# Kernel optimization log

Hardware: AMD Instinct MI355X
Metric: run time of the kernel (lower is better)

## Reference

```python
import jax, jax.numpy as jnp
import numpy as np
import math

B, T = 2, 1024
D_MODEL = 1024
N_HEAD = 16
HEAD_DIM = D_MODEL // N_HEAD
VOCAB = 32000
NUM_LOOP = 4
EPS_LN = 1e-5                       # torch LayerNorm default
EPS_RMS = float(np.finfo(np.float32).eps)  # torch RMSNorm eps=None -> finfo eps


def setup_inputs() -> dict:
    key = jax.random.key(0)
    ks = jax.random.split(key, 12)
    s = 0.02
    d = D_MODEL
    tok = jax.random.normal(ks[1], (VOCAB, d), jnp.float32) * s
    tok = tok.at[0].set(0.0)  # padding_idx=0
    return {
        "idx": jax.random.randint(ks[0], (B, T), 0, VOCAB),
        "tok_embed": tok,
        "ln_e_g": jnp.ones((d,), jnp.float32),
        "ln_e_b": jnp.zeros((d,), jnp.float32),
        "Wqkv": jax.random.normal(ks[2], (d, 3 * d), jnp.float32) * s,
        "bqkv": jnp.zeros((3 * d,), jnp.float32),
        "Wo": jax.random.normal(ks[3], (d, d), jnp.float32) * s,
        "bo": jnp.zeros((d,), jnp.float32),
        "W1": jax.random.normal(ks[4], (d, 4 * d), jnp.float32) * s,
        "b1": jnp.zeros((4 * d,), jnp.float32),
        "W2": jax.random.normal(ks[5], (4 * d, d), jnp.float32) * s,
        "b2": jnp.zeros((d,), jnp.float32),
        "n1_w": jnp.ones((d,), jnp.float32),
        "n2_w": jnp.ones((d,), jnp.float32),
        "lnf_g": jnp.ones((d,), jnp.float32),
        "lnf_b": jnp.zeros((d,), jnp.float32),
        "Wlm": jax.random.normal(ks[6], (d, VOCAB), jnp.float32) * s,
        "blm": jnp.zeros((VOCAB,), jnp.float32),
    }


def layernorm(x, g, b):
    m = jnp.mean(x, axis=-1, keepdims=True)
    v = jnp.mean(jnp.square(x - m), axis=-1, keepdims=True)
    return (x - m) * jax.lax.rsqrt(v + EPS_LN) * g + b


def rmsnorm(x, w):
    ms = jnp.mean(jnp.square(x), axis=-1, keepdims=True)
    return x * jax.lax.rsqrt(ms + EPS_RMS) * w


def gelu_tanh(x):
    c = math.sqrt(2.0 / math.pi)
    return 0.5 * x * (1.0 + jnp.tanh(c * (x + 0.044715 * x * x * x)))


def alibi_causal_bias(t):
    # rpe[q,k] = -(q-k) for q>k else 0, scaled per head by 2^(-8/H*(h+1)); causal -inf above diag
    pos = jnp.arange(t)
    rel = pos[:, None] - pos[None, :]                      # [T,T] = q - k
    slopes = 2.0 ** (-8.0 / N_HEAD * jnp.arange(1, N_HEAD + 1, dtype=jnp.float32))
    bias = -slopes[:, None, None] * rel.astype(jnp.float32)  # [H,T,T]
    return jnp.where(rel[None] >= 0, bias, -jnp.inf)       # causal mask fused


def reference(idx, tok_embed, ln_e_g, ln_e_b, Wqkv, bqkv, Wo, bo,
              W1, b1, W2, b2, n1_w, n2_w, lnf_g, lnf_b, Wlm, blm):
    b, t = idx.shape
    x = layernorm(tok_embed[idx], ln_e_g, ln_e_b)          # rpe=True: no sinusoidal PE
    bias = alibi_causal_bias(t)                            # [H,T,T]
    scale = 1.0 / math.sqrt(HEAD_DIM)

    for _ in range(NUM_LOOP):
        # attention sublayer
        h = rmsnorm(x, n1_w)
        qkv = h @ Wqkv + bqkv
        q, k, v = jnp.split(qkv, 3, axis=-1)
        q = q.reshape(b, t, N_HEAD, HEAD_DIM).transpose(0, 2, 1, 3)
        k = k.reshape(b, t, N_HEAD, HEAD_DIM).transpose(0, 2, 1, 3)
        v = v.reshape(b, t, N_HEAD, HEAD_DIM).transpose(0, 2, 1, 3)
        att = jnp.einsum('bhqd,bhkd->bhqk', q, k) * scale + bias[None]
        att = jax.nn.softmax(att, axis=-1)
        y = jnp.einsum('bhqk,bhkd->bhqd', att, v)
        y = y.transpose(0, 2, 1, 3).reshape(b, t, D_MODEL)
        x = x + (y @ Wo + bo)
        # mlp sublayer
        h = rmsnorm(x, n2_w)
        x = x + (gelu_tanh(h @ W1 + b1) @ W2 + b2)

    x = layernorm(x, lnf_g, lnf_b)
    return x @ Wlm + blm  # [B,T,VOCAB]
```

## Files before the change

### kernel.cpp

```cpp
#include <hip/hip_runtime.h>
#include <stdint.h>

#define DEVI __device__ __forceinline__

typedef __attribute__((ext_vector_type(8))) short short8;
typedef __attribute__((ext_vector_type(4))) float f32x4;
typedef unsigned short u16;
typedef unsigned int u32;

typedef const __attribute__((address_space(1))) void* gas_ptr;
typedef __attribute__((address_space(3))) void* las_ptr;

constexpr int BBATCH = 2;
constexpr int TT  = 1024;
constexpr int BT  = BBATCH * TT;
constexpr int DM  = 1024;
constexpr int NH  = 16;
constexpr int HD  = 64;
constexpr int DFF = 4096;
constexpr int NV  = 32000;
constexpr int NL  = 4;

DEVI u16 f2b(float f) {
  u32 u = __builtin_bit_cast(u32, f);
  u = (u + 0x7fffu + ((u >> 16) & 1u)) >> 16;
  return (u16)u;
}
DEVI float b2f(u16 h) { return __builtin_bit_cast(float, (u32)h << 16); }

DEVI void gld16(const void* g, void* l) {
  __builtin_amdgcn_global_load_lds((gas_ptr)g, (las_ptr)l, 16, 0, 0);
}

DEVI float wave_sum(float v) {
#pragma unroll
  for (int off = 32; off; off >>= 1) v += __shfl_xor(v, off);
  return v;
}
DEVI float block_sum(float v, float* sb) {
  v = wave_sum(v);
  int lane = threadIdx.x & 63, wid = threadIdx.x >> 6;
  __syncthreads();
  if (lane == 0) sb[wid] = v;
  __syncthreads();
  return sb[0] + sb[1] + sb[2] + sb[3];
}

DEVI float gelu_f(float x) {
  float u = 0.7978845608028654f * (x + 0.044715f * x * x * x);
  float e = __expf(2.0f * u);
  return x * (1.0f - 1.0f / (e + 1.0f));
}

__global__ __launch_bounds__(256) void wt_transpose_all(
    const float* __restrict__ Wqkv, const float* __restrict__ Wo,
    const float* __restrict__ W1, const float* __restrict__ W2,
    const float* __restrict__ Wlm,
    u16* __restrict__ WqkvT, u16* __restrict__ WoT, u16* __restrict__ W1T,
    u16* __restrict__ W2T, u16* __restrict__ WlmT) {
  __shared__ float t[64][33];
  int bid = blockIdx.x;
  const float* in; u16* out; int K, N, tt;
  if (bid < 1536)      { in = Wqkv; out = WqkvT; K = 1024; N = 3072;  tt = bid; }
  else if (bid < 2048) { in = Wo;   out = WoT;   K = 1024; N = 1024;  tt = bid - 1536; }
  else if (bid < 4096) { in = W1;   out = W1T;   K = 1024; N = 4096;  tt = bid - 2048; }
  else if (bid < 6144) { in = W2;   out = W2T;   K = 4096; N = 1024;  tt = bid - 4096; }
  else                 { in = Wlm;  out = WlmT;  K = 1024; N = 32000; tt = bid - 6144; }
  int nx = N >> 5;
  int n0 = (tt % nx) * 32, k0 = (tt / nx) * 64;
  int tx = threadIdx.x & 31, ty = threadIdx.x >> 5;
#pragma unroll
  for (int i = 0; i < 8; ++i)
    t[ty + 8 * i][tx] = in[(size_t)(k0 + ty + 8 * i) * N + n0 + tx];
  __syncthreads();
#pragma unroll
  for (int i = 0; i < 4; ++i) {
    int r = ty + 8 * i;
    u32 pk = (u32)f2b(t[2 * tx][r]) | ((u32)f2b(t[2 * tx + 1][r]) << 16);
    *(u32*)(out + (size_t)(n0 + r) * K + k0 + 2 * tx) = pk;
  }
}

__global__ __launch_bounds__(256) void embed_ln_k(const int* __restrict__ idx,
                                                  const float* __restrict__ tok,
                                                  const float* __restrict__ g,
                                                  const float* __restrict__ b,
                                                  float* __restrict__ x) {
  __shared__ float sb[4];
  int row = blockIdx.x, tid = threadIdx.x;
  float4 v = ((const float4*)(tok + (size_t)idx[row] * DM))[tid];
  float s = block_sum(v.x + v.y + v.z + v.w, sb);
  float m = s * (1.0f / DM);
  float dx = v.x - m, dy = v.y - m, dz = v.z - m, dw = v.w - m;
  float q = block_sum(dx * dx + dy * dy + dz * dz + dw * dw, sb);
  float rs = rsqrtf(q * (1.0f / DM) + 1e-5f);
  float4 gg = ((const float4*)g)[tid];
  float4 bb = ((const float4*)b)[tid];
  float4 o = make_float4(dx * rs * gg.x + bb.x, dy * rs * gg.y + bb.y,
                         dz * rs * gg.z + bb.z, dw * rs * gg.w + bb.w);
  ((float4*)(x + (size_t)row * DM))[tid] = o;
}

__global__ __launch_bounds__(256) void final_ln_k(const float* __restrict__ x,
                                                  const float* __restrict__ g,
                                                  const float* __restrict__ b,
                                                  u16* __restrict__ xf) {
  __shared__ float sb[4];
  int row = blockIdx.x, tid = threadIdx.x;
  float4 v = ((const float4*)(x + (size_t)row * DM))[tid];
  float s = block_sum(v.x + v.y + v.z + v.w, sb);
  float m = s * (1.0f / DM);
  float dx = v.x - m, dy = v.y - m, dz = v.z - m, dw = v.w - m;
  float q = block_sum(dx * dx + dy * dy + dz * dz + dw * dw, sb);
  float rs = rsqrtf(q * (1.0f / DM) + 1e-5f);
  float4 gg = ((const float4*)g)[tid];
  float4 bb = ((const float4*)b)[tid];
  u32 lo = (u32)f2b(dx * rs * gg.x + bb.x) | ((u32)f2b(dy * rs * gg.y + bb.y) << 16);
  u32 hi = (u32)f2b(dz * rs * gg.z + bb.z) | ((u32)f2b(dw * rs * gg.w + bb.w) << 16);
  ((uint2*)(xf + (size_t)row * DM))[tid] = make_uint2(lo, hi);
}

__global__ __launch_bounds__(256) void rmsnorm_k(const float* __restrict__ x,
                                                 const float* __restrict__ w,
                                                 u16* __restrict__ h) {
  __shared__ float sb[4];
  int row = blockIdx.x, tid = threadIdx.x;
  float4 v = ((const float4*)(x + (size_t)row * DM))[tid];
  float q = block_sum(v.x * v.x + v.y * v.y + v.z * v.z + v.w * v.w, sb);
  float rs = rsqrtf(q * (1.0f / DM) + 1.1920928955078125e-7f);
  float4 ww = ((const float4*)w)[tid];
  u32 lo = (u32)f2b(v.x * rs * ww.x) | ((u32)f2b(v.y * rs * ww.y) << 16);
  u32 hi = (u32)f2b(v.z * rs * ww.z) | ((u32)f2b(v.w * rs * ww.w) << 16);
  ((uint2*)(h + (size_t)row * DM))[tid] = make_uint2(lo, hi);
}

__global__ __launch_bounds__(256) void attn_k(const u16* __restrict__ qkv,
                                              const u16* __restrict__ vT,
                                              u16* __restrict__ y) {
  __shared__ __align__(16) char sP[16384];
  __shared__ __align__(16) char sK[2][16384];
  __shared__ __align__(16) char sV[2][16384];
  const int tid = threadIdx.x, lane = tid & 63, wid = tid >> 6;
  const int bid = blockIdx.x;
  const int sl = (bid + (bid >> 8)) & 15;
  const int qt = (sl & 1) ? (sl >> 1) : (15 - (sl >> 1));
  const int bh = (bid >> 4) & 31, b = bh >> 4, h = bh & 15;
  const int nt = (qt >> 1) + 1;
  const float slope = exp2f(-0.5f * (float)(h + 1));

  const char* Qb = (const char*)(qkv + (size_t)b * TT * 3 * DM + h * HD);
  const char* Kb = (const char*)(qkv + (size_t)b * TT * 3 * DM + DM + h * HD);
  const char* Vb = (const char*)(vT + (size_t)bh * HD * TT);

#pragma unroll
  for (int ci = 0; ci < 2; ++ci) {
    int c = wid * 2 + ci;
    int r = c * 8 + (lane >> 3);
    int q = (lane & 7) ^ (r & 7);
    gld16(Qb + (size_t)(qt * 64 + r) * 6144 + q * 16, sP + c * 1024 + lane * 16);
  }

  auto stageKV = [&](int buf, int kt) {
    int kv0 = kt * 128;
#pragma unroll
    for (int ci = 0; ci < 4; ++ci) {
      int c = wid * 4 + ci;
      int r = c * 8 + (lane >> 3);
      int q = (lane & 7) ^ (r & 7);
      gld16(Kb + (size_t)(kv0 + r) * 6144 + q * 16, sK[buf] + c * 1024 + lane * 16);
    }
#pragma unroll
    for (int ci = 0; ci < 4; ++ci) {
      int c = wid * 4 + ci;
      int d = c * 4 + (lane >> 4);
      int q = (lane & 15) ^ (d & 15);
      gld16(Vb + (size_t)d * 2048 + (size_t)kv0 * 2 + q * 16, sV[buf] + c * 1024 + lane * 16);
    }
  };
  stageKV(0, 0);
  asm volatile("s_waitcnt vmcnt(8)" ::: "memory");

  short8 qf[2];
#pragma unroll
  for (int ks = 0; ks < 2; ++ks) {
    int r = wid * 16 + (lane & 15);
    int q = ((ks << 2) + (lane >> 4)) ^ (r & 7);
    qf[ks] = *(const short8*)(sP + r * 128 + q * 16);
  }

  f32x4 Y[4] = {};
  float m_r[4], l_r[4];
#pragma unroll
  for (int r = 0; r < 4; ++r) { m_r[r] = -3e38f; l_r[r] = 0.0f; }

  for (int kt = 0; kt < nt; ++kt) {
    const int cur = kt & 1;
    if (kt + 1 < nt) {
      stageKV(cur ^ 1, kt + 1);
      asm volatile("s_waitcnt vmcnt(8)" ::: "memory");
    } else {
      asm volatile("s_waitcnt vmcnt(0)" ::: "memory");
    }
    __syncthreads();

    f32x4 s[8] = {};
    __builtin_amdgcn_s_setprio(1);
#pragma unroll
    for (int ks = 0; ks < 2; ++ks) {
      short8 kf[8];
#pragma unroll
      for (int j = 0; j < 8; ++j) {
        int r = j * 16 + (lane & 15);
        int q = ((ks << 2) + (lane >> 4)) ^ (r & 7);
        kf[j] = *(const short8*)(sK[cur] + r * 128 + q * 16);
      }
#pragma unroll
      for (int j = 0; j < 8; ++j)
        s[j] = __builtin_amdgcn_mfma_f32_16x16x32_bf16(qf[ks], kf[j], s[j], 0, 0, 0);
    }
    __builtin_amdgcn_s_setprio(0);

    const int kv0 = kt * 128;
    const int qbase = qt * 64 + wid * 16 + ((lane >> 4) << 2);
    float colb[8];
#pragma unroll
    for (int j = 0; j < 8; ++j)
      colb[j] = slope * (float)(kv0 + j * 16 + (lane & 15));
    float rowmax[4] = {-3e38f, -3e38f, -3e38f, -3e38f};
    if (kv0 + 127 <= qt * 64) {
#pragma unroll
      for (int j = 0; j < 8; ++j)
#pragma unroll
        for (int r = 0; r < 4; ++r) {
          float v = fmaf(s[j][r], 0.125f, colb[j]);
          s[j][r] = v;
          rowmax[r] = fmaxf(rowmax[r], v);
        }
    } else {
#pragma unroll
      for (int j = 0; j < 8; ++j) {
        int kcol = kv0 + j * 16 + (lane & 15);
#pragma unroll
        for (int r = 0; r < 4; ++r) {
          float v = (kcol <= qbase + r) ? fmaf(s[j][r], 0.125f, colb[j]) : -3e38f;
          s[j][r] = v;
          rowmax[r] = fmaxf(rowmax[r], v);
        }
      }
    }
#pragma unroll
    for (int r = 0; r < 4; ++r) {
      rowmax[r] = fmaxf(rowmax[r], __shfl_xor(rowmax[r], 1));
      rowmax[r] = fmaxf(rowmax[r], __shfl_xor(rowmax[r], 2));
      rowmax[r] = fmaxf(rowmax[r], __shfl_xor(rowmax[r], 4));
      rowmax[r] = fmaxf(rowmax[r], __shfl_xor(rowmax[r], 8));
      float mn = fmaxf(m_r[r], rowmax[r]);
      float al = __expf(m_r[r] - mn);
      m_r[r] = mn;
      l_r[r] *= al;
#pragma unroll
      for (int j = 0; j < 4; ++j) Y[j][r] *= al;
    }
    float rs[4] = {0.0f, 0.0f, 0.0f, 0.0f};
#pragma unroll
    for (int j = 0; j < 8; ++j)
#pragma unroll
      for (int r = 0; r < 4; ++r) {
        float p = __expf(s[j][r] - m_r[r]);
        s[j][r] = p;
        rs[r] += p;
      }
#pragma unroll
    for (int r = 0; r < 4; ++r) {
      rs[r] += __shfl_xor(rs[r], 1);
      rs[r] += __shfl_xor(rs[r], 2);
      rs[r] += __shfl_xor(rs[r], 4);
      rs[r] += __shfl_xor(rs[r], 8);
      l_r[r] += rs[r];
    }
#pragma unroll
    for (int j = 0; j < 8; ++j)
#pragma unroll
      for (int r = 0; r < 4; ++r) {
        int rl = wid * 16 + ((lane >> 4) << 2) + r;
        int c = j * 16 + (lane & 15);
        int g = c >> 3;
        *(u16*)(sP + rl * 256 + ((g ^ (rl & 15)) << 4) + (c & 7) * 2) = f2b(s[j][r]);
      }

    __builtin_amdgcn_s_setprio(1);
#pragma unroll
    for (int ks = 0; ks < 4; ++ks) {
      short8 pf, vf[4];
      {
        int r = wid * 16 + (lane & 15);
        int q = ((ks << 2) + (lane >> 4)) ^ (r & 15);
        pf = *(const short8*)(sP + r * 256 + (q << 4));
      }
#pragma unroll
      for (int j = 0; j < 4; ++j) {
        int d = j * 16 + (lane & 15);
        int q = ((ks << 2) + (lane >> 4)) ^ (d & 15);
        vf[j] = *(const short8*)(sV[cur] + d * 256 + (q << 4));
      }
#pragma unroll
      for (int j = 0; j < 4; ++j)
        Y[j] = __builtin_amdgcn_mfma_f32_16x16x32_bf16(pf, vf[j], Y[j], 0, 0, 0);
    }
    __builtin_amdgcn_s_setprio(0);
    __syncthreads();
  }

#pragma unroll
  for (int r = 0; r < 4; ++r) {
    float inv = 1.0f / l_r[r];
    int qrow = qt * 64 + wid * 16 + ((lane >> 4) << 2) + r;
    u16* yp = y + (size_t)(b * TT + qrow) * DM + h * HD;
#pragma unroll
    for (int j = 0; j < 4; ++j)
      yp[j * 16 + (lane & 15)] = f2b(Y[j][r] * inv);
  }
}

enum { EPI_BF16 = 0, EPI_GELU = 1, EPI_ADDF32 = 2, EPI_F32 = 3, EPI_ATOMIC = 4, EPI_QKV = 5 };

template <int BM, int BN, int WM, int WN, int EPI, int KS = 1>
__global__ __launch_bounds__(256, 2) void gemm_bt(
    const u16* __restrict__ A, int lda, const u16* __restrict__ Bt, int ldb,
    const float* __restrict__ bias, void* __restrict__ C, int ldc,
    float* __restrict__ resid, int K, u16* __restrict__ vTout) {
  constexpr int BK = 64;
  constexpr int NW = WM * WN;
  constexpr int FM = BM / WM / 16, FN = BN / WN / 16;
  constexpr int ABYTES = BM * BK * 2, BBYTES = BN * BK * 2;
  constexpr int ACH = ABYTES / 1024, BCH = BBYTES / 1024, NCH = ACH + BCH;
  extern __shared__ __align__(16) char smem[];

  const int tid = threadIdx.x, lane = tid & 63, wid = tid >> 6;
  const int brow = blockIdx.y * BM, bcol = blockIdx.x * BN;
  const long long kbase2 = (long long)blockIdx.z * (K / KS) * 2;

  const int nt = (K / KS) >> 6;
  const int widm = wid / WN, widn = wid % WN;
  const int rm0 = widm * (BM / WM), cn0 = widn * (BN / WN);

  f32x4 acc[FM][FN] = {};

  const int swq16 = (((lane & 7) ^ ((lane >> 3) & 7)) << 4);
  const int lrow8 = lane >> 3;

  auto stage = [&](int buf, int kt) {
    char* base = smem + buf * (ABYTES + BBYTES);
    const char* Ag = (const char*)A;
    const char* Bg = (const char*)Bt;
    long long kOff = kbase2 + (long long)kt * 128 + swq16;
#pragma unroll
    for (int ci = 0; ci < NCH / NW; ++ci) {
      int c = wid + ci * NW;
      if (c < ACH) {
        int r = c * 8 + lrow8;
        gld16(Ag + (long long)(brow + r) * (lda * 2) + kOff, base + c * 1024 + lane * 16);
      } else {
        int r = (c - ACH) * 8 + lrow8;
        gld16(Bg + (long long)(bcol + r) * (ldb * 2) + kOff,
              base + ABYTES + (c - ACH) * 1024 + lane * 16);
      }
    }
  };

  auto compute = [&](int buf) {
    char* baseA = smem + buf * (ABYTES + BBYTES);
    char* baseB = baseA + ABYTES;
#pragma unroll
    for (int ks = 0; ks < 2; ++ks) {
      short8 af[FM], bv[FN];
#pragma unroll
      for (int i = 0; i < FM; ++i) {
        int r = rm0 + i * 16 + (lane & 15);
        int cq = ((ks << 2) + (lane >> 4)) ^ (r & 7);
        af[i] = *(const short8*)(baseA + r * 128 + (cq << 4));
      }
#pragma unroll
      for (int j = 0; j < FN; ++j) {
        int r = cn0 + j * 16 + (lane & 15);
        int cq = ((ks << 2) + (lane >> 4)) ^ (r & 7);
        bv[j] = *(const short8*)(baseB + r * 128 + (cq << 4));
      }
#pragma unroll
      for (int i = 0; i < FM; ++i)
#pragma unroll
        for (int j = 0; j < FN; ++j)
          acc[i][j] = __builtin_amdgcn_mfma_f32_16x16x32_bf16(af[i], bv[j], acc[i][j], 0, 0, 0);
    }
  };

  stage(0, 0);
  __syncthreads();
  int cur = 0;
  for (int t = 0; t < nt; ++t) {
    if (t + 1 < nt) stage(cur ^ 1, t + 1);
    compute(cur);
    __syncthreads();
    cur ^= 1;
  }

  if constexpr (EPI == EPI_QKV) {
    if (bcol >= 2 * DM) {
      u16* st = (u16*)smem;
#pragma unroll
      for (int i = 0; i < FM; ++i)
#pragma unroll
        for (int j = 0; j < FN; ++j)
#pragma unroll
          for (int r = 0; r < 4; ++r) {
            int rl = rm0 + i * 16 + ((lane >> 4) << 2) + r;
            int cl = cn0 + j * 16 + (lane & 15);
            st[rl * 130 + cl] = f2b(acc[i][j][r] + bias[bcol + cl]);
          }
      __syncthreads();
      const int b = brow >> 10, t0b = brow & (TT - 1);
      const int h0 = (bcol - 2 * DM) >> 6;
      constexpr int NCHK = BM / 8;
      constexpr int DPP = 256 / NCHK;
      const int sub = tid & (NCHK - 1);
#pragma unroll
      for (int pass = 0; pass < 128 / DPP; ++pass) {
        int d = pass * DPP + (tid / NCHK);
        u32 pk[4];
#pragma unroll
        for (int k2 = 0; k2 < 4; ++k2) {
          u16 lo = st[(sub * 8 + 2 * k2) * 130 + d];
          u16 hi = st[(sub * 8 + 2 * k2 + 1) * 130 + d];
          pk[k2] = (u32)lo | ((u32)hi << 16);
        }
        int head = h0 + (d >> 6), dd = d & 63;
        *(uint4*)(vTout + ((size_t)((b * NH + head) * HD + dd)) * TT + t0b + sub * 8) =
            make_uint4(pk[0], pk[1], pk[2], pk[3]);
      }
      return;
    }
  }

  const int r0 = brow + rm0 + ((lane >> 4) << 2);
  const int c0 = bcol + cn0 + (lane & 15);
#pragma unroll
  for (int i = 0; i < FM; ++i) {
#pragma unroll
    for (int j = 0; j < FN; ++j) {
#pragma unroll
      for (int r = 0; r < 4; ++r) {
        int row = r0 + i * 16 + r;
        int col = c0 + j * 16;
        float v = acc[i][j][r];
        if constexpr (EPI == EPI_BF16 || EPI == EPI_QKV) {
          ((u16*)C)[(size_t)row * ldc + col] = f2b(v + bias[col]);
        } else if constexpr (EPI == EPI_GELU) {
          ((u16*)C)[(size_t)row * ldc + col] = f2b(gelu_f(v + bias[col]));
        } else if constexpr (EPI == EPI_ADDF32) {
          size_t o = (size_t)row * ldc + col;
          resid[o] += v + bias[col];
        } else if constexpr (EPI == EPI_ATOMIC) {
          size_t o = (size_t)row * ldc + col;
          atomicAdd(&resid[o], v + (blockIdx.z == 0 ? bias[col] : 0.0f));
        } else {
          ((float*)C)[(size_t)row * ldc + col] = v + bias[col];
        }
      }
    }
  }
}

template <int EPI>
__global__ __launch_bounds__(512, 2) void gemm8(
    const u16* __restrict__ A, int lda, const u16* __restrict__ Bt, int ldb,
    const float* __restrict__ bias, void* __restrict__ C, int ldc, int K, int nby) {
  __shared__ __align__(16) char smem[2][2][32768];
  const int tid = threadIdx.x, lane = tid & 63;
  const int wid = tid >> 6, wm = wid >> 2, wn = wid & 3;

  const int nb = gridDim.x;
  const int q8 = nb >> 3, r8 = nb & 7;
  const int xcd = blockIdx.x & 7, lin = blockIdx.x >> 3;
  const int idx = (xcd < r8 ? xcd * (q8 + 1) : r8 * (q8 + 1) + (xcd - r8) * q8) + lin;
  const int brow = (idx % nby) * 256, bcol = (idx / nby) * 256;

  const int nt = K >> 6, niter = nt >> 1;

  const int srow = tid >> 3, sq = tid & 7;
  auto stage = [&](int buf, int isB, int half, int kt) {
    const u16* G = isB ? Bt : A;
    const int ld = isB ? ldb : lda;
    const int base = isB ? bcol : brow;
    char* L = &smem[buf][isB][half * 16384];
#pragma unroll
    for (int l = 0; l < 2; ++l) {
      int rl = half * 128 + l * 64 + srow;
      gld16((const char*)G + (size_t)(base + rl) * (ld * 2) + kt * 128 + ((sq ^ (rl & 7)) << 4),
            L + l * 8192 + tid * 16);
    }
  };

  short8 bfr[4][2], afr[2][2];
  f32x4 acc[8][4] = {};

  stage(0, 0, 0, 0); stage(0, 0, 1, 0);
  stage(0, 1, 0, 0); stage(0, 1, 1, 0);
  stage(1, 1, 0, 1); stage(1, 1, 1, 1);
  asm volatile("s_waitcnt vmcnt(0)" ::: "memory");
  __builtin_amdgcn_s_barrier();

  for (int i = 0; i < niter; ++i) {
    const bool full = (i + 1 < niter);
    const int t2 = 2 * i + 2, t3 = 2 * i + 3;
#pragma unroll
    for (int h = 0; h < 2; ++h) {
#pragma unroll
      for (int qd = 0; qd < 4; ++qd) {
        if (qd == 0) {
#pragma unroll
          for (int j = 0; j < 4; ++j)
#pragma unroll
            for (int ks = 0; ks < 2; ++ks) {
              int r = wn * 64 + j * 16 + (lane & 15);
              int q = ((ks << 2) + (lane >> 4)) ^ (r & 7);
              bfr[j][ks] = *(const short8*)&smem[h][1][r * 128 + q * 16];
            }
        }
#pragma unroll
        for (int f = 0; f < 2; ++f)
#pragma unroll
          for (int ks = 0; ks < 2; ++ks) {
            int r = wm * 128 + (qd * 2 + f) * 16 + (lane & 15);
            int q = ((ks << 2) + (lane >> 4)) ^ (r & 7);
            afr[f][ks] = *(const short8*)&smem[h][0][r * 128 + q * 16];
          }
        if (h == 0) {
          if (qd == 0) stage(1, 0, 0, 2 * i + 1);
          else if (qd == 1) stage(1, 0, 1, 2 * i + 1);
          else if (qd == 2) { if (full) stage(0, 1, 0, t2); }
          else              { if (full) stage(0, 1, 1, t2); }
        } else {
          if (qd == 0)      { if (full) stage(0, 0, 0, t2); }
          else if (qd == 1) { if (full) stage(0, 0, 1, t2); }
          else if (qd == 2) { if (full) stage(1, 1, 0, t3); }
          else              { if (full) stage(1, 1, 1, t3); }
        }
        if (qd == 3) {
          if (full) asm volatile("s_waitcnt vmcnt(4)" ::: "memory");
          else if (h == 0) asm volatile("s_waitcnt vmcnt(0)" ::: "memory");
        }
        __builtin_amdgcn_s_barrier();
        asm volatile("s_waitcnt lgkmcnt(0)" ::: "memory");
        __builtin_amdgcn_s_setprio(1);
#pragma unroll
        for (int f = 0; f < 2; ++f)
#pragma unroll
          for (int j = 0; j < 4; ++j)
#pragma unroll
            for (int ks = 0; ks < 2; ++ks)
              acc[qd * 2 + f][j] = __builtin_amdgcn_mfma_f32_16x16x32_bf16(
                  afr[f][ks], bfr[j][ks], acc[qd * 2 + f][j], 0, 0, 0);
        __builtin_amdgcn_s_setprio(0);
        __builtin_amdgcn_s_barrier();
      }
    }
  }

  const int r0 = brow + wm * 128 + ((lane >> 4) << 2);
  const int c0 = bcol + wn * 64 + (lane & 15);
#pragma unroll
  for (int fi = 0; fi < 8; ++fi) {
#pragma unroll
    for (int j = 0; j < 4; ++j) {
      int col = c0 + j * 16;
      float bv = bias[col];
#pragma unroll
      for (int r = 0; r < 4; ++r) {
        int row = r0 + fi * 16 + r;
        float v = acc[fi][j][r] + bv;
        if constexpr (EPI == EPI_F32)
          ((float*)C)[(size_t)row * ldc + col] = v;
        else if constexpr (EPI == EPI_GELU)
          ((u16*)C)[(size_t)row * ldc + col] = f2b(gelu_f(v));
        else
          ((u16*)C)[(size_t)row * ldc + col] = f2b(v);
      }
    }
  }
}

extern "C" void kernel_launch(void* const* d_in, const int* in_sizes, int n_in,
                              void* d_out, int out_size, void* d_ws, size_t ws_size,
                              hipStream_t stream) {
  (void)in_sizes; (void)n_in; (void)out_size;
  const int*   idx    = (const int*)d_in[0];
  const float* tok    = (const float*)d_in[1];
  const float* ln_e_g = (const float*)d_in[2];
  const float* ln_e_b = (const float*)d_in[3];
  const float* Wqkv   = (const float*)d_in[4];
  const float* bqkv   = (const float*)d_in[5];
  const float* Wo     = (const float*)d_in[6];
  const float* bo     = (const float*)d_in[7];
  const float* W1     = (const float*)d_in[8];
  const float* b1     = (const float*)d_in[9];
  const float* W2     = (const float*)d_in[10];
  const float* b2     = (const float*)d_in[11];
  const float* n1_w   = (const float*)d_in[12];
  const float* n2_w   = (const float*)d_in[13];
  const float* lnf_g  = (const float*)d_in[14];
  const float* lnf_b  = (const float*)d_in[15];
  const float* Wlm    = (const float*)d_in[16];
  const float* blm    = (const float*)d_in[17];
  float* out = (float*)d_out;

  char* w = (char*)d_ws;
  auto alloc = [&](size_t bytes) { char* p = w; w += (bytes + 255) & ~(size_t)255; return p; };
  float* x   = (float*)alloc((size_t)BT * DM * 4);
  u16* h     = (u16*)alloc((size_t)BT * DM * 2);
  u16* qkv   = (u16*)alloc((size_t)BT * 3 * DM * 2);
  u16* vT    = (u16*)alloc((size_t)BBATCH * NH * HD * TT * 2);
  u16* y     = (u16*)alloc((size_t)BT * DM * 2);
  u16* act   = (u16*)alloc((size_t)BT * DFF * 2);
  u16* xf    = (u16*)alloc((size_t)BT * DM * 2);
  u16* WqkvT = (u16*)alloc((size_t)3 * DM * DM * 2);
  u16* WoT   = (u16*)alloc((size_t)DM * DM * 2);
  u16* W1T   = (u16*)alloc((size_t)DFF * DM * 2);
  u16* W2T   = (u16*)alloc((size_t)DM * DFF * 2);
  u16* WlmT  = (u16*)alloc((size_t)NV * DM * 2);
  if ((size_t)(w - (char*)d_ws) > ws_size) return;

  wt_transpose_all<<<22144, 256, 0, stream>>>(Wqkv, Wo, W1, W2, Wlm,
                                              WqkvT, WoT, W1T, W2T, WlmT);

  embed_ln_k<<<BT, 256, 0, stream>>>(idx, tok, ln_e_g, ln_e_b, x);

  constexpr int SM128 = 2 * (128 * 64 * 2 + 128 * 64 * 2);
  constexpr int SM64  = 2 * (128 * 64 * 2 + 64 * 64 * 2);
  constexpr int SMQ   = 2 * (64 * 64 * 2 + 128 * 64 * 2);

  for (int l = 0; l < NL; ++l) {
    rmsnorm_k<<<BT, 256, 0, stream>>>(x, n1_w, h);
    gemm_bt<64, 128, 2, 2, EPI_QKV><<<dim3(3 * DM / 128, BT / 64), 256, SMQ, stream>>>(
        h, DM, WqkvT, DM, bqkv, qkv, 3 * DM, nullptr, DM, vT);
    attn_k<<<512, 256, 0, stream>>>(qkv, vT, y);
    gemm_bt<128, 64, 4, 1, EPI_ADDF32><<<dim3(DM / 64, BT / 128), 256, SM64, stream>>>(
        y, DM, WoT, DM, bo, nullptr, DM, x, DM, nullptr);
    rmsnorm_k<<<BT, 256, 0, stream>>>(x, n2_w, h);
    gemm_bt<128, 128, 2, 2, EPI_GELU><<<dim3(DFF / 128, BT / 128), 256, SM128, stream>>>(
        h, DM, W1T, DM, b1, act, DFF, nullptr, DM, nullptr);
    gemm_bt<128, 128, 2, 2, EPI_ATOMIC, 2><<<dim3(DM / 128, BT / 128, 2), 256, SM128, stream>>>(
        act, DFF, W2T, DFF, b2, nullptr, DM, x, DFF, nullptr);
  }

  final_ln_k<<<BT, 256, 0, stream>>>(x, lnf_g, lnf_b, xf);
  gemm8<EPI_F32><<<dim3((NV / 256) * (BT / 256)), 512, 0, stream>>>(
      xf, DM, WlmT, DM, blm, out, NV, DM, BT / 256);
}
```

Measured before the change: 814.6 us.

## Add triple-buffered GEMM pipeline for QKV/Wo and fuse embed-LN into transpose kernel

Adds a 3-stage shared-memory pipeline option to gemm_bt that keeps two tiles in flight, using vmcnt waits and one barrier per iteration. It is enabled for the QKV and output-projection GEMMs, which have short K loops. The embedding layernorm is also folded into the weight-transpose launch as extra blocks, removing one kernel launch. Risks: the hard-coded vmcnt(6) must match the number of loads issued per stage, and the larger shared-memory footprint may reduce occupancy.

```diff
diff --git a/kernel.cpp b/kernel.cpp
--- a/kernel.cpp
+++ b/kernel.cpp
@@ -52,14 +52,33 @@
   return x * (1.0f - 1.0f / (e + 1.0f));
 }
 
-__global__ __launch_bounds__(256) void wt_transpose_all(
+__global__ __launch_bounds__(256) void wt_embed_all(
     const float* __restrict__ Wqkv, const float* __restrict__ Wo,
     const float* __restrict__ W1, const float* __restrict__ W2,
     const float* __restrict__ Wlm,
     u16* __restrict__ WqkvT, u16* __restrict__ WoT, u16* __restrict__ W1T,
-    u16* __restrict__ W2T, u16* __restrict__ WlmT) {
+    u16* __restrict__ W2T, u16* __restrict__ WlmT,
+    const int* __restrict__ idx, const float* __restrict__ tok,
+    const float* __restrict__ ln_g, const float* __restrict__ ln_b,
+    float* __restrict__ x) {
   __shared__ float t[64][33];
   int bid = blockIdx.x;
+  if (bid >= 22144) {
+    int row = bid - 22144, tid = threadIdx.x;
+    float* sb = &t[0][0];
+    float4 v = ((const float4*)(tok + (size_t)idx[row] * DM))[tid];
+    float s = block_sum(v.x + v.y + v.z + v.w, sb);
+    float m = s * (1.0f / DM);
+    float dx = v.x - m, dy = v.y - m, dz = v.z - m, dw = v.w - m;
+    float q = block_sum(dx * dx + dy * dy + dz * dz + dw * dw, sb);
+    float rs = rsqrtf(q * (1.0f / DM) + 1e-5f);
+    float4 gg = ((const float4*)ln_g)[tid];
+    float4 bb = ((const float4*)ln_b)[tid];
+    float4 o = make_float4(dx * rs * gg.x + bb.x, dy * rs * gg.y + bb.y,
+                           dz * rs * gg.z + bb.z, dw * rs * gg.w + bb.w);
+    ((float4*)(x + (size_t)row * DM))[tid] = o;
+    return;
+  }
   const float* in; u16* out; int K, N, tt;
   if (bid < 1536)      { in = Wqkv; out = WqkvT; K = 1024; N = 3072;  tt = bid; }
   else if (bid < 2048) { in = Wo;   out = WoT;   K = 1024; N = 1024;  tt = bid - 1536; }
@@ -79,26 +98,6 @@
     u32 pk = (u32)f2b(t[2 * tx][r]) | ((u32)f2b(t[2 * tx + 1][r]) << 16);
     *(u32*)(out + (size_t)(n0 + r) * K + k0 + 2 * tx) = pk;
   }
-}
-
-__global__ __launch_bounds__(256) void embed_ln_k(const int* __restrict__ idx,
-                                                  const float* __restrict__ tok,
-                                                  const float* __restrict__ g,
-                                                  const float* __restrict__ b,
-                                                  float* __restrict__ x) {
-  __shared__ float sb[4];
-  int row = blockIdx.x, tid = threadIdx.x;
-  float4 v = ((const float4*)(tok + (size_t)idx[row] * DM))[tid];
-  float s = block_sum(v.x + v.y + v.z + v.w, sb);
-  float m = s * (1.0f / DM);
-  float dx = v.x - m, dy = v.y - m, dz = v.z - m, dw = v.w - m;
-  float q = block_sum(dx * dx + dy * dy + dz * dz + dw * dw, sb);
-  float rs = rsqrtf(q * (1.0f / DM) + 1e-5f);
-  float4 gg = ((const float4*)g)[tid];
-  float4 bb = ((const float4*)b)[tid];
-  float4 o = make_float4(dx * rs * gg.x + bb.x, dy * rs * gg.y + bb.y,
-                         dz * rs * gg.z + bb.z, dw * rs * gg.w + bb.w);
-  ((float4*)(x + (size_t)row * DM))[tid] = o;
 }
 
 __global__ __launch_bounds__(256) void final_ln_k(const float* __restrict__ x,
@@ -324,7 +323,7 @@
 
 enum { EPI_BF16 = 0, EPI_GELU = 1, EPI_ADDF32 = 2, EPI_F32 = 3, EPI_ATOMIC = 4, EPI_QKV = 5 };
 
-template <int BM, int BN, int WM, int WN, int EPI, int KS = 1>
+template <int BM, int BN, int WM, int WN, int EPI, int KS = 1, int STAGES = 2>
 __global__ __launch_bounds__(256, 2) void gemm_bt(
     const u16* __restrict__ A, int lda, const u16* __restrict__ Bt, int ldb,
     const float* __restrict__ bias, void* __restrict__ C, int ldc,
@@ -394,14 +393,27 @@
     }
   };
 
-  stage(0, 0);
-  __syncthreads();
-  int cur = 0;
-  for (int t = 0; t < nt; ++t) {
-    if (t + 1 < nt) stage(cur ^ 1, t + 1);
-    compute(cur);
+  if constexpr (STAGES == 3) {
+    stage(0, 0);
+    if (1 < nt) stage(1, 1);
+    for (int t = 0; t < nt; ++t) {
+      if (t + 1 < nt) asm volatile("s_waitcnt vmcnt(6)" ::: "memory");
+      else            asm volatile("s_waitcnt vmcnt(0)" ::: "memory");
+      __syncthreads();
+      if (t + 2 < nt) stage((t + 2) % 3, t + 2);
+      compute(t % 3);
+    }
     __syncthreads();
-    cur ^= 1;
+  } else {
+    stage(0, 0);
+    __syncthreads();
+    int cur = 0;
+    for (int t = 0; t < nt; ++t) {
+      if (t + 1 < nt) stage(cur ^ 1, t + 1);
+      compute(cur);
+      __syncthreads();
+      cur ^= 1;
+    }
   }
 
   if constexpr (EPI == EPI_QKV) {
@@ -629,21 +641,20 @@
   u16* WlmT  = (u16*)alloc((size_t)NV * DM * 2);
   if ((size_t)(w - (char*)d_ws) > ws_size) return;
 
-  wt_transpose_all<<<22144, 256, 0, stream>>>(Wqkv, Wo, W1, W2, Wlm,
-                                              WqkvT, WoT, W1T, W2T, WlmT);
-
-  embed_ln_k<<<BT, 256, 0, stream>>>(idx, tok, ln_e_g, ln_e_b, x);
+  wt_embed_all<<<22144 + BT, 256, 0, stream>>>(Wqkv, Wo, W1, W2, Wlm,
+                                               WqkvT, WoT, W1T, W2T, WlmT,
+                                               idx, tok, ln_e_g, ln_e_b, x);
 
   constexpr int SM128 = 2 * (128 * 64 * 2 + 128 * 64 * 2);
-  constexpr int SM64  = 2 * (128 * 64 * 2 + 64 * 64 * 2);
-  constexpr int SMQ   = 2 * (64 * 64 * 2 + 128 * 64 * 2);
+  constexpr int SM64_3 = 3 * (128 * 64 * 2 + 64 * 64 * 2);
+  constexpr int SMQ3   = 3 * (64 * 64 * 2 + 128 * 64 * 2);
 
   for (int l = 0; l < NL; ++l) {
     rmsnorm_k<<<BT, 256, 0, stream>>>(x, n1_w, h);
-    gemm_bt<64, 128, 2, 2, EPI_QKV><<<dim3(3 * DM / 128, BT / 64), 256, SMQ, stream>>>(
+    gemm_bt<64, 128, 2, 2, EPI_QKV, 1, 3><<<dim3(3 * DM / 128, BT / 64), 256, SMQ3, stream>>>(
         h, DM, WqkvT, DM, bqkv, qkv, 3 * DM, nullptr, DM, vT);
     attn_k<<<512, 256, 0, stream>>>(qkv, vT, y);
-    gemm_bt<128, 64, 4, 1, EPI_ADDF32><<<dim3(DM / 64, BT / 128), 256, SM64, stream>>>(
+    gemm_bt<128, 64, 4, 1, EPI_ADDF32, 1, 3><<<dim3(DM / 64, BT / 128), 256, SM64_3, stream>>>(
         y, DM, WoT, DM, bo, nullptr, DM, x, DM, nullptr);
     rmsnorm_k<<<BT, 256, 0, stream>>>(x, n2_w, h);
     gemm_bt<128, 128, 2, 2, EPI_GELU><<<dim3(DFF / 128, BT / 128), 256, SM128, stream>>>(
```

After: 829.9 us. Within noise of the previous version (+1.9%).
